# Performance work log

Hardware: AMD Instinct MI355X
Metric: run time of the kernel (lower is better)

Reference implementation:

```python
import jax, jax.numpy as jnp
import numpy as np

N = 32768; D = 384; P = 3; CORR_D = 2 * 49 * P * P  # 882
G_KK = 4096; G_JK = 512
EPS = 1e-3  # LayerNorm eps in the torch module

FLOAT_NAMES = ("net","inp","corr","corr_w1","corr_b1","corr_w2","corr_b2","corr_ln_g","corr_ln_b","corr_w3","corr_b3","norm_g","norm_b","c1_w1","c1_b1","c1_w2","c1_b2","c2_w1","c2_b1","c2_w2","c2_b2","kk_fw","kk_fb","kk_gw","kk_gb","kk_hw","kk_hb","ij_fw","ij_fb","ij_gw","ij_gb","ij_hw","ij_hb","g_ln1_g","g_ln1_b","g1_gw","g1_gb","g1_r1w","g1_r1b","g1_r2w","g1_r2b","g_ln2_g","g_ln2_b","g2_gw","g2_gb","g2_r1w","g2_r1b","g2_r2w","g2_r2b","d_w","d_b","w_w","w_b")

def _ln(x, g, b):
    m = jnp.mean(x, -1, keepdims=True)
    v = jnp.mean((x - m) ** 2, -1, keepdims=True)
    return (x - m) * jax.lax.rsqrt(v + EPS) * g + b

def _mlp2(x, w1, b1, w2, b2):
    return jax.nn.relu(x @ w1 + b1) @ w2 + b2

def _gated_residual(x, gw, gb, r1w, r1b, r2w, r2b):
    gate = jax.nn.sigmoid(x @ gw + gb)
    res = jax.nn.relu(x @ r1w + r1b) @ r2w + r2b
    return x + gate * res

def _soft_agg(x, jx, fw, fb, gw, gb, hw, hb, num_groups):
    # x: [N, D]; jx: [N] group ids -> group-wise softmax weighted sum
    logits = x @ gw + gb
    feats = x @ fw + fb
    gmax = jax.ops.segment_max(logits, jx, num_segments=num_groups)
    e = jnp.exp(logits - gmax[jx])
    den = jax.ops.segment_sum(e, jx, num_segments=num_groups)
    w = e / (den[jx] + 1e-12)
    y = jax.ops.segment_sum(feats * w, jx, num_segments=num_groups)
    return (y @ hw + hb)[jx]

def _forward(p, nix, njx, ukk, ujk):
    # corr encoder MLP
    h = jax.nn.relu(p["corr"] @ p["corr_w1"] + p["corr_b1"]) @ p["corr_w2"] + p["corr_b2"]
    h = jax.nn.relu(_ln(h, p["corr_ln_g"], p["corr_ln_b"])) @ p["corr_w3"] + p["corr_b3"]
    net = p["net"] + p["inp"] + h
    net = _ln(net, p["norm_g"], p["norm_b"])
    mask_ix = (nix >= 0).astype(net.dtype).reshape(1, -1, 1)
    mask_jx = (njx >= 0).astype(net.dtype).reshape(1, -1, 1)
    net = net + _mlp2(mask_ix * net[:, nix], p["c1_w1"], p["c1_b1"], p["c1_w2"], p["c1_b2"])
    net = net + _mlp2(mask_jx * net[:, njx], p["c2_w1"], p["c2_b1"], p["c2_w2"], p["c2_b2"])
    net = net + _soft_agg(net[0], ukk, p["kk_fw"], p["kk_fb"], p["kk_gw"], p["kk_gb"], p["kk_hw"], p["kk_hb"], G_KK)[None]
    net = net + _soft_agg(net[0], ujk, p["ij_fw"], p["ij_fb"], p["ij_gw"], p["ij_gb"], p["ij_hw"], p["ij_hb"], G_JK)[None]
    net = _ln(net, p["g_ln1_g"], p["g_ln1_b"])
    net = _gated_residual(net, p["g1_gw"], p["g1_gb"], p["g1_r1w"], p["g1_r1b"], p["g1_r2w"], p["g1_r2b"])
    net = _ln(net, p["g_ln2_g"], p["g_ln2_b"])
    net = _gated_residual(net, p["g2_gw"], p["g2_gb"], p["g2_r1w"], p["g2_r1b"], p["g2_r2w"], p["g2_r2b"])
    r = jax.nn.relu(net)
    d = r @ p["d_w"] + p["d_b"]               # GradClip is identity in forward
    w = jax.nn.sigmoid(r @ p["w_w"] + p["w_b"])
    return net, d, w

def setup_inputs() -> dict:
    key = jax.random.key(0)
    it = iter(jax.random.split(key, 64))
    def pr(*shape):
        return jax.random.normal(next(it), shape, dtype=jnp.float32) * 0.02
    z = lambda *s: jnp.zeros(s, jnp.float32)
    o = lambda *s: jnp.ones(s, jnp.float32)
    inp = {
        "net": jax.random.normal(next(it), (1, N, D), dtype=jnp.float32),
        "inp": jax.random.normal(next(it), (1, N, D), dtype=jnp.float32),
        "corr": jax.random.normal(next(it), (1, N, CORR_D), dtype=jnp.float32),
        "nix": jax.random.randint(next(it), (N,), 0, N),
        "njx": jax.random.randint(next(it), (N,), 0, N),
        "ukk": jax.random.randint(next(it), (N,), 0, G_KK),
        "ujk": jax.random.randint(next(it), (N,), 0, G_JK),
        "corr_w1": pr(CORR_D, D), "corr_b1": z(D), "corr_w2": pr(D, D), "corr_b2": z(D),
        "corr_ln_g": o(D), "corr_ln_b": z(D), "corr_w3": pr(D, D), "corr_b3": z(D),
        "norm_g": o(D), "norm_b": z(D),
        "c1_w1": pr(D, D), "c1_b1": z(D), "c1_w2": pr(D, D), "c1_b2": z(D),
        "c2_w1": pr(D, D), "c2_b1": z(D), "c2_w2": pr(D, D), "c2_b2": z(D),
        "kk_fw": pr(D, D), "kk_fb": z(D), "kk_gw": pr(D, D), "kk_gb": z(D), "kk_hw": pr(D, D), "kk_hb": z(D),
        "ij_fw": pr(D, D), "ij_fb": z(D), "ij_gw": pr(D, D), "ij_gb": z(D), "ij_hw": pr(D, D), "ij_hb": z(D),
        "g_ln1_g": o(D), "g_ln1_b": z(D),
        "g1_gw": pr(D, D), "g1_gb": z(D), "g1_r1w": pr(D, D), "g1_r1b": z(D), "g1_r2w": pr(D, D), "g1_r2b": z(D),
        "g_ln2_g": o(D), "g_ln2_b": z(D),
        "g2_gw": pr(D, D), "g2_gb": z(D), "g2_r1w": pr(D, D), "g2_r1b": z(D), "g2_r2w": pr(D, D), "g2_r2b": z(D),
        "d_w": pr(D, 2), "d_b": z(2), "w_w": pr(D, 2), "w_b": z(2),
    }
    return inp

def reference(net, inp, corr, corr_w1, corr_b1, corr_w2, corr_b2, corr_ln_g, corr_ln_b, corr_w3, corr_b3, norm_g, norm_b, c1_w1, c1_b1, c1_w2, c1_b2, c2_w1, c2_b1, c2_w2, c2_b2, kk_fw, kk_fb, kk_gw, kk_gb, kk_hw, kk_hb, ij_fw, ij_fb, ij_gw, ij_gb, ij_hw, ij_hb, g_ln1_g, g_ln1_b, g1_gw, g1_gb, g1_r1w, g1_r1b, g1_r2w, g1_r2b, g_ln2_g, g_ln2_b, g2_gw, g2_gb, g2_r1w, g2_r1b, g2_r2w, g2_r2b, d_w, d_b, w_w, w_b, nix, njx, ukk, ujk):
    loc = locals()
    fl = {k: loc[k] for k in FLOAT_NAMES}
    return _forward(fl, nix, njx, ukk, ujk)
```

## Files before the change

### kernel.cpp

```cpp
#include <hip/hip_runtime.h>
#include <hip/hip_bf16.h>
#include <math.h>

#define NR 32768
#define DD 384
#define CDM 882
#define CDMP 896

typedef float f4 __attribute__((ext_vector_type(4)));
typedef float f32x4 __attribute__((ext_vector_type(4)));
typedef __bf16 bf16x8 __attribute__((ext_vector_type(8)));
typedef __bf16 bf16x4 __attribute__((ext_vector_type(4)));

__device__ inline f4 ld4(const float* p) { f4 v; __builtin_memcpy(&v, p, 16); return v; }
__device__ inline void st4(float* p, f4 v) { __builtin_memcpy(p, &v, 16); }
__device__ inline bf16x8 ld8h(const __bf16* p) { bf16x8 v; __builtin_memcpy(&v, p, 16); return v; }
__device__ inline void st8h(__bf16* p, bf16x8 v) { __builtin_memcpy(p, &v, 16); }

__device__ inline void gl_lds16(const void* g, void* l) {
  __builtin_amdgcn_global_load_lds(
      (const __attribute__((address_space(1))) void*)g,
      (__attribute__((address_space(3))) void*)l, 16, 0, 0);
}

__device__ inline float gred16(float v) {
#pragma unroll
  for (int o = 1; o < 16; o <<= 1) v += __shfl_xor(v, o, 64);
  return v;
}

struct WPtrs { const float* w[18]; };

__global__ __launch_bounds__(256) void trans_all_k(WPtrs P, __bf16* __restrict__ dst) {
  int wi = blockIdx.y;
  const float* W = P.w[wi];
  __bf16* WT = dst + (size_t)wi * DD * DD;
  int i = blockIdx.x * 256 + threadIdx.x;
  if (i >= DD * DD) return;
  int n = i / DD, k = i - n * DD;
  WT[i] = (__bf16)W[(size_t)k * DD + n];
}

__global__ __launch_bounds__(256) void trans_corr_k(const float* __restrict__ W,
                                                    __bf16* __restrict__ WT) {
  int i = blockIdx.x * 256 + threadIdx.x;
  if (i >= DD * CDMP) return;
  int n = i / CDMP, k = i - n * CDMP;
  WT[i] = (k < CDM) ? (__bf16)W[(size_t)k * DD + n] : (__bf16)0.f;
}

template <int EPI, int AFP32>
__global__ __launch_bounds__(256, 2) void gemm_k(
    const void* __restrict__ Av, const __bf16* __restrict__ WT,
    const float* __restrict__ bias, __bf16* __restrict__ OUT,
    const __bf16* __restrict__ XRES, const int* __restrict__ idx,
    const __bf16* __restrict__ zpage, int M, int K, int Kreal, int nwg) {
  __shared__ __align__(16) __bf16 sm[2][2][128 * 64];
  const int t = threadIdx.x;
  const int w = t >> 6, lane = t & 63;
  int orig = blockIdx.x;
  int q = nwg >> 3, r = nwg & 7, xcd = orig & 7, lid = orig >> 3;
  int wg = (xcd < r ? xcd * (q + 1) : r * (q + 1) + (xcd - r) * q) + lid;
  const int m0 = (wg / 3) * 128;
  const int n0 = (wg % 3) * 128;
  const int fr = lane & 15, fq = lane >> 4;
  const int wr = (w >> 1) * 64, wc = (w & 1) * 64;

  const __bf16* bptr[4];
  const __bf16* aptr[4];
  int aadv[4];
#pragma unroll
  for (int j = 0; j < 4; ++j) {
    int rloc = w * 32 + j * 8 + (lane >> 3);
    int cch = (lane & 7) ^ (rloc & 7);
    bptr[j] = WT + (size_t)(n0 + rloc) * K + cch * 8;
    if constexpr (!AFP32) {
      int gm = m0 + rloc;
      int ar = idx ? idx[gm] : gm;
      if (ar >= 0) { aptr[j] = (const __bf16*)Av + (size_t)ar * K + cch * 8; aadv[j] = 64; }
      else { aptr[j] = zpage; aadv[j] = 0; }
    }
  }
  const float* Af = (const float*)Av;
  const int NT = K >> 6;

  f32x4 acc[4][4];
#pragma unroll
  for (int a = 0; a < 4; ++a)
#pragma unroll
    for (int b = 0; b < 4; ++b)
#pragma unroll
      for (int j = 0; j < 4; ++j) acc[a][b][j] = 0.f;

  auto stage = [&](int buf, int k0) {
    __bf16* As = sm[buf][0];
    __bf16* Bs = sm[buf][1];
    if constexpr (AFP32) {
#pragma unroll
      for (int p = 0; p < 4; ++p) {
        int rr = p * 32 + (t >> 3);
        int cc = t & 7;
        int kb = k0 + cc * 8;
        const float* ap = Af + (size_t)(m0 + rr) * Kreal + kb;
        float vv[8];
        if (kb + 8 <= Kreal) {
          f4 v0 = ld4(ap), v1 = ld4(ap + 4);
#pragma unroll
          for (int e = 0; e < 4; ++e) { vv[e] = v0[e]; vv[4 + e] = v1[e]; }
        } else {
#pragma unroll
          for (int e = 0; e < 8; ++e) vv[e] = (kb + e < Kreal) ? ap[e] : 0.f;
        }
        bf16x8 h;
#pragma unroll
        for (int e = 0; e < 8; ++e) h[e] = (__bf16)vv[e];
        *reinterpret_cast<bf16x8*>(&As[rr * 64 + (((cc ^ (rr & 7)) << 3))]) = h;
      }
    } else {
#pragma unroll
      for (int j = 0; j < 4; ++j) {
        gl_lds16(aptr[j], &As[(w * 32 + j * 8) * 64]);
        aptr[j] += aadv[j];
      }
    }
#pragma unroll
    for (int j = 0; j < 4; ++j) {
      gl_lds16(bptr[j], &Bs[(w * 32 + j * 8) * 64]);
      bptr[j] += 64;
    }
  };

  auto compute = [&](int buf) {
    const __bf16* As = sm[buf][0];
    const __bf16* Bs = sm[buf][1];
#pragma unroll
    for (int kk2 = 0; kk2 < 2; ++kk2) {
      bf16x8 af[4], bv[4];
#pragma unroll
      for (int mi = 0; mi < 4; ++mi) {
        int rr = wr + mi * 16 + fr;
        af[mi] = *reinterpret_cast<const bf16x8*>(
            &As[rr * 64 + (((fq + kk2 * 4) ^ (rr & 7)) << 3)]);
      }
#pragma unroll
      for (int ni = 0; ni < 4; ++ni) {
        int rr = wc + ni * 16 + fr;
        bv[ni] = *reinterpret_cast<const bf16x8*>(
            &Bs[rr * 64 + (((fq + kk2 * 4) ^ (rr & 7)) << 3)]);
      }
#pragma unroll
      for (int mi = 0; mi < 4; ++mi)
#pragma unroll
        for (int ni = 0; ni < 4; ++ni)
          acc[mi][ni] = __builtin_amdgcn_mfma_f32_16x16x32_bf16(af[mi], bv[ni],
                                                                acc[mi][ni], 0, 0, 0);
    }
  };

  stage(0, 0);
  __syncthreads();
  int cur = 0;
  for (int tt = 0; tt < NT; ++tt) {
    if (tt + 1 < NT) stage(cur ^ 1, (tt + 1) << 6);
    compute(cur);
    __syncthreads();
    cur ^= 1;
  }

#pragma unroll
  for (int mi = 0; mi < 4; ++mi)
#pragma unroll
    for (int ni = 0; ni < 4; ++ni) {
      int col = n0 + wc + ni * 16 + fr;
      float bvv = bias[col];
#pragma unroll
      for (int j = 0; j < 4; ++j) {
        int row = m0 + wr + mi * 16 + fq * 4 + j;
        size_t o = (size_t)row * DD + col;
        float v = acc[mi][ni][j] + bvv;
        if constexpr (EPI == 0) {
          OUT[o] = (__bf16)v;
        } else if constexpr (EPI == 1) {
          OUT[o] = (__bf16)fmaxf(v, 0.f);
        } else if constexpr (EPI == 2) {
          OUT[o] = (__bf16)((float)OUT[o] + v);
        } else {
          float gl = (float)OUT[o];
          float g = 1.f / (1.f + expf(-gl));
          OUT[o] = (__bf16)((float)XRES[o] + g * v);
        }
      }
    }
}

template <int RELU>
__global__ __launch_bounds__(256) void ln_k(const __bf16* __restrict__ x,
                                            const float* __restrict__ g,
                                            const float* __restrict__ b,
                                            __bf16* __restrict__ out) {
  int w = threadIdx.x >> 6, lane = threadIdx.x & 63;
  int s = lane & 15, qq = lane >> 4;
  int row = blockIdx.x * 16 + w * 4 + qq;
  size_t base = (size_t)row * DD;
  float v[24];
#pragma unroll
  for (int i = 0; i < 3; ++i) {
    bf16x8 h = ld8h(x + base + (s + 16 * i) * 8);
#pragma unroll
    for (int e = 0; e < 8; ++e) v[i * 8 + e] = (float)h[e];
  }
  float sm = 0.f;
#pragma unroll
  for (int i = 0; i < 24; ++i) sm += v[i];
  sm = gred16(sm);
  float mean = sm * (1.f / 384.f);
  float qs = 0.f;
#pragma unroll
  for (int i = 0; i < 24; ++i) { float d = v[i] - mean; qs += d * d; }
  qs = gred16(qs);
  float rs = rsqrtf(qs * (1.f / 384.f) + 1e-3f);
#pragma unroll
  for (int i = 0; i < 3; ++i) {
    int col = (s + 16 * i) * 8;
    f4 g0 = ld4(g + col), g1 = ld4(g + col + 4);
    f4 b0 = ld4(b + col), b1 = ld4(b + col + 4);
    bf16x8 o;
#pragma unroll
    for (int e = 0; e < 4; ++e) {
      float y0 = (v[i * 8 + e] - mean) * rs * g0[e] + b0[e];
      float y1 = (v[i * 8 + 4 + e] - mean) * rs * g1[e] + b1[e];
      if (RELU) { y0 = fmaxf(y0, 0.f); y1 = fmaxf(y1, 0.f); }
      o[e] = (__bf16)y0; o[4 + e] = (__bf16)y1;
    }
    st8h(out + base + col, o);
  }
}

__global__ __launch_bounds__(256) void ln3_k(const float* __restrict__ x1,
                                             const float* __restrict__ x2,
                                             const __bf16* __restrict__ x3,
                                             const float* __restrict__ g,
                                             const float* __restrict__ b,
                                             __bf16* __restrict__ out) {
  int w = threadIdx.x >> 6, lane = threadIdx.x & 63;
  int s = lane & 15, qq = lane >> 4;
  int row = blockIdx.x * 16 + w * 4 + qq;
  size_t base = (size_t)row * DD;
  float v[24];
#pragma unroll
  for (int i = 0; i < 3; ++i) {
    int col = (s + 16 * i) * 8;
    f4 a0 = ld4(x1 + base + col), a1 = ld4(x1 + base + col + 4);
    f4 c0 = ld4(x2 + base + col), c1 = ld4(x2 + base + col + 4);
    bf16x8 h = ld8h(x3 + base + col);
#pragma unroll
    for (int e = 0; e < 4; ++e) {
      v[i * 8 + e] = a0[e] + c0[e] + (float)h[e];
      v[i * 8 + 4 + e] = a1[e] + c1[e] + (float)h[4 + e];
    }
  }
  float sm = 0.f;
#pragma unroll
  for (int i = 0; i < 24; ++i) sm += v[i];
  sm = gred16(sm);
  float mean = sm * (1.f / 384.f);
  float qs = 0.f;
#pragma unroll
  for (int i = 0; i < 24; ++i) { float d = v[i] - mean; qs += d * d; }
  qs = gred16(qs);
  float rs = rsqrtf(qs * (1.f / 384.f) + 1e-3f);
#pragma unroll
  for (int i = 0; i < 3; ++i) {
    int col = (s + 16 * i) * 8;
    f4 g0 = ld4(g + col), g1 = ld4(g + col + 4);
    f4 b0 = ld4(b + col), b1 = ld4(b + col + 4);
    bf16x8 o;
#pragma unroll
    for (int e = 0; e < 4; ++e) {
      o[e] = (__bf16)((v[i * 8 + e] - mean) * rs * g0[e] + b0[e]);
      o[4 + e] = (__bf16)((v[i * 8 + 4 + e] - mean) * rs * g1[e] + b1[e]);
    }
    st8h(out + base + col, o);
  }
}

__global__ __launch_bounds__(256) void hist_k(const int* __restrict__ gid,
                                              int* __restrict__ cnt, int n) {
  int i = blockIdx.x * 256 + threadIdx.x;
  if (i < n) atomicAdd(&cnt[gid[i]], 1);
}

__global__ __launch_bounds__(256) void scan_k(const int* __restrict__ cnt,
                                              int* __restrict__ off, int G) {
  __shared__ int ls[256];
  int t = threadIdx.x;
  int per = G / 256;
  int base = t * per;
  int s = 0;
  for (int i = 0; i < per; ++i) s += cnt[base + i];
  ls[t] = s;
  __syncthreads();
  for (int o = 1; o < 256; o <<= 1) {
    int v = (t >= o) ? ls[t - o] : 0;
    __syncthreads();
    ls[t] += v;
    __syncthreads();
  }
  int run = (t == 0) ? 0 : ls[t - 1];
  for (int i = 0; i < per; ++i) {
    off[base + i] = run;
    run += cnt[base + i];
  }
  if (t == 255) off[G] = run;
}

__global__ __launch_bounds__(256) void scatter_k(const int* __restrict__ gid,
                                                 const int* __restrict__ off,
                                                 int* __restrict__ cur,
                                                 int* __restrict__ rows, int n) {
  int i = blockIdx.x * 256 + threadIdx.x;
  if (i >= n) return;
  int g = gid[i];
  int p = atomicAdd(&cur[g], 1);
  rows[off[g] + p] = i;
}

__global__ __launch_bounds__(384) void segagg_k(const __bf16* __restrict__ L,
                                                const __bf16* __restrict__ Ft,
                                                const int* __restrict__ rows,
                                                const int* __restrict__ off,
                                                float* __restrict__ yb) {
  int g = blockIdx.x;
  int c = threadIdx.x;
  int s = off[g], e = off[g + 1];
  float mx = -3.0e38f;
  for (int p = s; p < e; ++p) {
    int r = rows[p];
    mx = fmaxf(mx, (float)L[(size_t)r * DD + c]);
  }
  float num = 0.f, den = 0.f;
  for (int p = s; p < e; ++p) {
    int r = rows[p];
    float lv = (float)L[(size_t)r * DD + c];
    float fv = (float)Ft[(size_t)r * DD + c];
    float ev = expf(lv - mx);
    den += ev;
    num += fv * ev;
  }
  yb[(size_t)g * DD + c] = num / (den + 1e-12f);
}

__global__ __launch_bounds__(256) void addgather_k(__bf16* __restrict__ X,
                                                   const __bf16* __restrict__ z,
                                                   const int* __restrict__ gid) {
  int i = blockIdx.x * 256 + threadIdx.x;
  int row = i / 48, c = (i - row * 48) * 8;
  int g = gid[row];
  size_t lo = (size_t)row * DD + c;
  bf16x8 a = ld8h(X + lo);
  bf16x8 zz = ld8h(z + (size_t)g * DD + c);
  bf16x8 o;
#pragma unroll
  for (int e = 0; e < 8; ++e) o[e] = (__bf16)((float)a[e] + (float)zz[e]);
  st8h(X + lo, o);
}

__global__ __launch_bounds__(256) void final_k(const __bf16* __restrict__ net,
                                               const float* __restrict__ dw,
                                               const float* __restrict__ db,
                                               const float* __restrict__ ww,
                                               const float* __restrict__ wb,
                                               float* __restrict__ out) {
  int w = threadIdx.x >> 6, lane = threadIdx.x & 63;
  int s = lane & 15, qq = lane >> 4;
  int row = blockIdx.x * 16 + w * 4 + qq;
  size_t base = (size_t)row * DD;
  float d0 = 0, d1 = 0, w0 = 0, w1 = 0;
#pragma unroll
  for (int i = 0; i < 3; ++i) {
    int col = (s + 16 * i) * 8;
    bf16x8 h = ld8h(net + base + col);
    f4 o0, o1;
#pragma unroll
    for (int e = 0; e < 4; ++e) {
      float x0 = (float)h[e], x1 = (float)h[4 + e];
      o0[e] = x0; o1[e] = x1;
      float r0 = fmaxf(x0, 0.f), r1 = fmaxf(x1, 0.f);
      int c0 = col + e, c1 = col + 4 + e;
      d0 += r0 * dw[2 * c0] + r1 * dw[2 * c1];
      d1 += r0 * dw[2 * c0 + 1] + r1 * dw[2 * c1 + 1];
      w0 += r0 * ww[2 * c0] + r1 * ww[2 * c1];
      w1 += r0 * ww[2 * c0 + 1] + r1 * ww[2 * c1 + 1];
    }
    st4(out + base + col, o0);
    st4(out + base + col + 4, o1);
  }
  d0 = gred16(d0); d1 = gred16(d1); w0 = gred16(w0); w1 = gred16(w1);
  if (s == 0) {
    float* outd = out + (size_t)NR * DD;
    float* outw = outd + (size_t)NR * 2;
    outd[2 * row] = d0 + db[0];
    outd[2 * row + 1] = d1 + db[1];
    outw[2 * row] = 1.f / (1.f + expf(-(w0 + wb[0])));
    outw[2 * row + 1] = 1.f / (1.f + expf(-(w1 + wb[1])));
  }
}

extern "C" void kernel_launch(void* const* d_in, const int* in_sizes, int n_in,
                              void* d_out, int out_size, void* d_ws, size_t ws_size,
                              hipStream_t stream) {
  const float* in_net = (const float*)d_in[0];
  const float* in_inp = (const float*)d_in[1];
  const float* in_corr = (const float*)d_in[2];
  const int* nix = (const int*)d_in[3];
  const int* njx = (const int*)d_in[4];
  const int* ukk = (const int*)d_in[5];
  const int* ujk = (const int*)d_in[6];
  auto F = [&](int i) { return (const float*)d_in[i]; };

  constexpr size_t SZ_ACT = (size_t)NR * DD * 2;
  char* ws = (char*)d_ws;
  __bf16* T1b = (__bf16*)(ws);
  __bf16* T2b = (__bf16*)(ws + SZ_ACT);
  __bf16* Fb = (__bf16*)(ws + 2 * SZ_ACT);
  __bf16* zb = (__bf16*)(ws + 3 * SZ_ACT);
  char* p = ws + 3 * SZ_ACT + 4ull * 1024 * 1024;
  float* yb = (float*)p; p += (size_t)4096 * DD * 4;
  int* rows = (int*)p; p += (size_t)NR * 4;
  int* off = (int*)p; p += 32768;
  int* cnt = (int*)p; p += 16384;
  int* curb = (int*)p; p += 16384;
  __bf16* wt_all = (__bf16*)p; p += (size_t)18 * DD * DD * 2;
  __bf16* wt_corr1 = (__bf16*)p; p += (size_t)DD * CDMP * 2;
  __bf16* zpage = (__bf16*)p;

  const int widx[18] = {17, 19, 21, 23, 25, 27, 29, 31, 33, 35, 39, 41, 43, 47, 49, 51, 9, 13};
  WPtrs P;
  for (int i = 0; i < 18; ++i) P.w[i] = F(widx[i]);
  auto WTp = [&](int i) { return wt_all + (size_t)i * DD * DD; };

  hipMemsetAsync(zpage, 0, 256, stream);
  trans_all_k<<<dim3(576, 18), 256, 0, stream>>>(P, wt_all);
  trans_corr_k<<<1344, 256, 0, stream>>>(F(7), wt_corr1);

  auto GEMM = [&](int epi, int afp32, const void* A, const __bf16* WT, const float* bias,
                  __bf16* OUT, const __bf16* XRES, const int* idx, int M, int Kp, int Kr) {
    int nwg = (M / 128) * 3;
    dim3 g(nwg), b(256);
    if (afp32) {
      if (epi == 1)
        gemm_k<1, 1><<<g, b, 0, stream>>>(A, WT, bias, OUT, XRES, idx, zpage, M, Kp, Kr, nwg);
      else
        gemm_k<0, 1><<<g, b, 0, stream>>>(A, WT, bias, OUT, XRES, idx, zpage, M, Kp, Kr, nwg);
    } else {
      switch (epi) {
        case 0: gemm_k<0, 0><<<g, b, 0, stream>>>(A, WT, bias, OUT, XRES, idx, zpage, M, Kp, Kr, nwg); break;
        case 1: gemm_k<1, 0><<<g, b, 0, stream>>>(A, WT, bias, OUT, XRES, idx, zpage, M, Kp, Kr, nwg); break;
        case 2: gemm_k<2, 0><<<g, b, 0, stream>>>(A, WT, bias, OUT, XRES, idx, zpage, M, Kp, Kr, nwg); break;
        default: gemm_k<3, 0><<<g, b, 0, stream>>>(A, WT, bias, OUT, XRES, idx, zpage, M, Kp, Kr, nwg); break;
      }
    }
  };

  auto SEGAGG = [&](const int* gid, int G, const __bf16* L, const __bf16* Ft) {
    hipMemsetAsync(cnt, 0, (size_t)G * 4, stream);
    hipMemsetAsync(curb, 0, (size_t)G * 4, stream);
    hist_k<<<NR / 256, 256, 0, stream>>>(gid, cnt, NR);
    scan_k<<<1, 256, 0, stream>>>(cnt, off, G);
    scatter_k<<<NR / 256, 256, 0, stream>>>(gid, off, curb, rows, NR);
    segagg_k<<<G, 384, 0, stream>>>(L, Ft, rows, off, yb);
  };

  const int LNG = NR / 16;
  const int SEGB = NR * 48 / 256;

  GEMM(1, 1, in_corr, wt_corr1, F(8), T1b, nullptr, nullptr, NR, CDMP, CDM);
  GEMM(0, 0, T1b, WTp(16), F(10), T2b, nullptr, nullptr, NR, DD, DD);
  ln_k<1><<<LNG, 256, 0, stream>>>(T2b, F(11), F(12), T1b);
  GEMM(0, 0, T1b, WTp(17), F(14), T2b, nullptr, nullptr, NR, DD, DD);
  ln3_k<<<LNG, 256, 0, stream>>>(in_net, in_inp, T2b, F(15), F(16), T1b);
  GEMM(1, 0, T1b, WTp(0), F(18), T2b, nullptr, nix, NR, DD, DD);
  GEMM(2, 0, T2b, WTp(1), F(20), T1b, nullptr, nullptr, NR, DD, DD);
  GEMM(1, 0, T1b, WTp(2), F(22), T2b, nullptr, njx, NR, DD, DD);
  GEMM(2, 0, T2b, WTp(3), F(24), T1b, nullptr, nullptr, NR, DD, DD);
  GEMM(0, 0, T1b, WTp(5), F(28), T2b, nullptr, nullptr, NR, DD, DD);
  GEMM(0, 0, T1b, WTp(4), F(26), Fb, nullptr, nullptr, NR, DD, DD);
  SEGAGG(ukk, 4096, T2b, Fb);
  GEMM(0, 1, yb, WTp(6), F(30), zb, nullptr, nullptr, 4096, DD, DD);
  addgather_k<<<SEGB, 256, 0, stream>>>(T1b, zb, ukk);
  GEMM(0, 0, T1b, WTp(8), F(34), T2b, nullptr, nullptr, NR, DD, DD);
  GEMM(0, 0, T1b, WTp(7), F(32), Fb, nullptr, nullptr, NR, DD, DD);
  SEGAGG(ujk, 512, T2b, Fb);
  GEMM(0, 1, yb, WTp(9), F(36), zb, nullptr, nullptr, 512, DD, DD);
  addgather_k<<<SEGB, 256, 0, stream>>>(T1b, zb, ujk);
  ln_k<0><<<LNG, 256, 0, stream>>>(T1b, F(37), F(38), T2b);
  GEMM(0, 0, T2b, WTp(10), F(40), Fb, nullptr, nullptr, NR, DD, DD);
  GEMM(1, 0, T2b, WTp(11), F(42), T1b, nullptr, nullptr, NR, DD, DD);
  GEMM(3, 0, T1b, WTp(12), F(44), Fb, T2b, nullptr, NR, DD, DD);
  ln_k<0><<<LNG, 256, 0, stream>>>(Fb, F(45), F(46), T1b);
  GEMM(0, 0, T1b, WTp(13), F(48), T2b, nullptr, nullptr, NR, DD, DD);
  GEMM(1, 0, T1b, WTp(14), F(50), Fb, nullptr, nullptr, NR, DD, DD);
  GEMM(3, 0, Fb, WTp(15), F(52), T2b, T1b, nullptr, NR, DD, DD);
  final_k<<<LNG, 256, 0, stream>>>(T2b, F(53), F(54), F(55), F(56), (float*)d_out);
}
```

Baseline: 742.4 us.

## Pre-convert corr input to bf16 and single-buffer GEMM LDS staging

Adds a kernel that converts the fp32 corr input to padded bf16 once, so the first GEMM can use the async global-to-LDS bf16 path instead of converting fp32 per tile. The GEMM drops LDS double buffering for a single buffer with two barriers per k-step, halving shared memory and possibly raising occupancy, but it no longer overlaps loads with MFMA work. The workspace layout is reshuffled so the converted input aliases a buffer written later.

```diff
diff --git a/kernel.cpp b/kernel.cpp
--- a/kernel.cpp
+++ b/kernel.cpp
@@ -27,6 +27,22 @@
 #pragma unroll
   for (int o = 1; o < 16; o <<= 1) v += __shfl_xor(v, o, 64);
   return v;
+}
+
+__global__ __launch_bounds__(256) void corr2bf16_k(const float* __restrict__ src,
+                                                   __bf16* __restrict__ dst) {
+  int i = blockIdx.x * 256 + threadIdx.x;
+  int row = i / 112, c8 = (i - row * 112) * 8;
+  const float* sp = src + (size_t)row * CDM + c8;
+  bf16x8 h;
+  if (c8 + 8 <= CDM) {
+#pragma unroll
+    for (int e = 0; e < 8; ++e) h[e] = (__bf16)sp[e];
+  } else {
+#pragma unroll
+    for (int e = 0; e < 8; ++e) h[e] = (c8 + e < CDM) ? (__bf16)sp[e] : (__bf16)0.f;
+  }
+  st8h(dst + (size_t)row * CDMP + c8, h);
 }
 
 struct WPtrs { const float* w[18]; };
@@ -55,7 +71,7 @@
     const float* __restrict__ bias, __bf16* __restrict__ OUT,
     const __bf16* __restrict__ XRES, const int* __restrict__ idx,
     const __bf16* __restrict__ zpage, int M, int K, int Kreal, int nwg) {
-  __shared__ __align__(16) __bf16 sm[2][2][128 * 64];
+  __shared__ __align__(16) __bf16 sm[2][128 * 64];
   const int t = threadIdx.x;
   const int w = t >> 6, lane = t & 63;
   int orig = blockIdx.x;
@@ -92,9 +108,9 @@
 #pragma unroll
       for (int j = 0; j < 4; ++j) acc[a][b][j] = 0.f;
 
-  auto stage = [&](int buf, int k0) {
-    __bf16* As = sm[buf][0];
-    __bf16* Bs = sm[buf][1];
+  auto stage = [&](int k0) {
+    __bf16* As = sm[0];
+    __bf16* Bs = sm[1];
     if constexpr (AFP32) {
 #pragma unroll
       for (int p = 0; p < 4; ++p) {
@@ -130,9 +146,9 @@
     }
   };
 
-  auto compute = [&](int buf) {
-    const __bf16* As = sm[buf][0];
-    const __bf16* Bs = sm[buf][1];
+  auto compute = [&]() {
+    const __bf16* As = sm[0];
+    const __bf16* Bs = sm[1];
 #pragma unroll
     for (int kk2 = 0; kk2 < 2; ++kk2) {
       bf16x8 af[4], bv[4];
@@ -157,14 +173,11 @@
     }
   };
 
-  stage(0, 0);
-  __syncthreads();
-  int cur = 0;
   for (int tt = 0; tt < NT; ++tt) {
-    if (tt + 1 < NT) stage(cur ^ 1, (tt + 1) << 6);
-    compute(cur);
+    if (tt) __syncthreads();
+    stage(tt << 6);
     __syncthreads();
-    cur ^= 1;
+    compute();
   }
 
 #pragma unroll
@@ -418,14 +431,16 @@
   const int* ujk = (const int*)d_in[6];
   auto F = [&](int i) { return (const float*)d_in[i]; };
 
+  constexpr size_t MiB = 1024 * 1024;
   constexpr size_t SZ_ACT = (size_t)NR * DD * 2;
   char* ws = (char*)d_ws;
-  __bf16* T1b = (__bf16*)(ws);
-  __bf16* T2b = (__bf16*)(ws + SZ_ACT);
-  __bf16* Fb = (__bf16*)(ws + 2 * SZ_ACT);
-  __bf16* zb = (__bf16*)(ws + 3 * SZ_ACT);
-  char* p = ws + 3 * SZ_ACT + 4ull * 1024 * 1024;
-  float* yb = (float*)p; p += (size_t)4096 * DD * 4;
+  __bf16* Xc = (__bf16*)(ws);
+  __bf16* T2b = (__bf16*)(ws);
+  __bf16* Fb = (__bf16*)(ws + SZ_ACT);
+  __bf16* zb = (__bf16*)(ws + 2 * SZ_ACT);
+  float* yb = (float*)(ws + 2 * SZ_ACT + 3 * MiB);
+  __bf16* T1b = (__bf16*)(ws + 60 * MiB);
+  char* p = ws + 84 * MiB;
   int* rows = (int*)p; p += (size_t)NR * 4;
   int* off = (int*)p; p += 32768;
   int* cnt = (int*)p; p += 16384;
@@ -442,16 +457,14 @@
   hipMemsetAsync(zpage, 0, 256, stream);
   trans_all_k<<<dim3(576, 18), 256, 0, stream>>>(P, wt_all);
   trans_corr_k<<<1344, 256, 0, stream>>>(F(7), wt_corr1);
+  corr2bf16_k<<<NR * 112 / 256, 256, 0, stream>>>(in_corr, Xc);
 
   auto GEMM = [&](int epi, int afp32, const void* A, const __bf16* WT, const float* bias,
                   __bf16* OUT, const __bf16* XRES, const int* idx, int M, int Kp, int Kr) {
     int nwg = (M / 128) * 3;
     dim3 g(nwg), b(256);
     if (afp32) {
-      if (epi == 1)
-        gemm_k<1, 1><<<g, b, 0, stream>>>(A, WT, bias, OUT, XRES, idx, zpage, M, Kp, Kr, nwg);
-      else
-        gemm_k<0, 1><<<g, b, 0, stream>>>(A, WT, bias, OUT, XRES, idx, zpage, M, Kp, Kr, nwg);
+      gemm_k<0, 1><<<g, b, 0, stream>>>(A, WT, bias, OUT, XRES, idx, zpage, M, Kp, Kr, nwg);
     } else {
       switch (epi) {
         case 0: gemm_k<0, 0><<<g, b, 0, stream>>>(A, WT, bias, OUT, XRES, idx, zpage, M, Kp, Kr, nwg); break;
@@ -474,7 +487,7 @@
   const int LNG = NR / 16;
   const int SEGB = NR * 48 / 256;
 
-  GEMM(1, 1, in_corr, wt_corr1, F(8), T1b, nullptr, nullptr, NR, CDMP, CDM);
+  GEMM(1, 0, Xc, wt_corr1, F(8), T1b, nullptr, nullptr, NR, CDMP, CDMP);
   GEMM(0, 0, T1b, WTp(16), F(10), T2b, nullptr, nullptr, NR, DD, DD);
   ln_k<1><<<LNG, 256, 0, stream>>>(T2b, F(11), F(12), T1b);
   GEMM(0, 0, T1b, WTp(17), F(14), T2b, nullptr, nullptr, NR, DD, DD);
```

Measured after the change: 656.4 us. 11.6% less time.
